# Performance work log

Measured on AMD Instinct MI355X. Metric: run time of the kernel, lower is better.

Reference implementation:

```python
import jax, jax.numpy as jnp
import numpy as np
from jax import lax

G = 64       # grid_size
K = 8        # N_knn
L = 64       # latent size
NP = 150000  # num points
NEG_SLOPE = 0.01


def lrelu(x):
    return jnp.where(x >= 0, x, NEG_SLOPE * x)


def setup_inputs() -> dict:
    key = jax.random.key(0)
    ks = jax.random.split(key, 16)
    inp = {
        "pc_KNN_pos": jax.random.normal(ks[0], (NP, K, 3), jnp.float32),
        "points": jax.random.randint(ks[1], (NP, 3), 0, G),
        # point MLP: 3 -> 64 -> 64 (LeakyReLU between)
        "W1": jax.random.normal(ks[2], (3, L), jnp.float32) * 0.3,
        "b1": jnp.zeros((L,), jnp.float32),
        "W2": jax.random.normal(ks[3], (L, L), jnp.float32) * 0.1,
        "b2": jnp.zeros((L,), jnp.float32),
        # knn aggregator: Conv1d(K,K,1) -> LeakyReLU -> Conv1d(K,1,1)
        "Wk1": jax.random.normal(ks[4], (K, K), jnp.float32) * 0.3,
        "bk1": jnp.zeros((K,), jnp.float32),
        "Wk2": jax.random.normal(ks[5], (1, K), jnp.float32) * 0.3,
        "bk2": jnp.zeros((1,), jnp.float32),
        "Cw1": jax.random.normal(ks[6], (L, L, 3, 3, 3), jnp.float32) * 0.02,
        "Cb1": jnp.zeros((L,), jnp.float32),
        "Cw2": jax.random.normal(ks[7], (L, L, 3, 3, 3), jnp.float32) * 0.02,
        "Cb2": jnp.zeros((L,), jnp.float32),
    }
    return inp


def reference(pc_KNN_pos, points, W1, b1, W2, b2, Wk1, bk1, Wk2, bk2, Cw1, Cb1, Cw2, Cb2):
    # point MLP over last dim: (Np, K, 3) -> (Np, K, L)
    h = lrelu(pc_KNN_pos @ W1 + b1)
    feat = h @ W2 + b2
    # knn_feat: 1x1 Conv1d over channel dim K (spatial dim = L)
    f1 = lrelu(jnp.einsum('ok,nkl->nol', Wk1, feat) + bk1[None, :, None])
    f2 = jnp.einsum('ok,nkl->nol', Wk2, f1) + bk2[None, :, None]  # (Np, 1, L)
    pfeat = f2[:, 0, :]  # (Np, L)
    # AvgPooling: scatter-average point features into G^3 grid cells
    idx = (points[:, 0] * G + points[:, 1]) * G + points[:, 2]  # (Np,)
    sums = jax.ops.segment_sum(pfeat, idx, num_segments=G * G * G)
    cnt = jax.ops.segment_sum(jnp.ones((pfeat.shape[0], 1), pfeat.dtype), idx,
                              num_segments=G * G * G)
    grid = jnp.where(cnt > 0, sums / jnp.maximum(cnt, 1.0), 0.0)
    grid = grid.reshape(G, G, G, L)
    # grid convs: (G,G,G,L) -> (1,L,G,G,G) -> convs -> (G,G,G,L)
    x = grid.transpose(3, 0, 1, 2)[None]
    dn = ('NCDHW', 'OIDHW', 'NCDHW')
    for w, b in ((Cw1, Cb1), (Cw2, Cb2)):
        x = lax.conv_general_dilated(x, w, (1, 1, 1), [(1, 1)] * 3,
                                     dimension_numbers=dn)
        x = jax.nn.relu(x + b[None, :, None, None, None])
    return x[0].transpose(1, 2, 3, 0)  # (G,G,G,L)
```

## Files before the change

### kernel.cpp

```cpp
#include <hip/hip_runtime.h>
#include <hip/hip_fp16.h>

#define G 64
#define KNN 8

typedef _Float16 f16x2 __attribute__((ext_vector_type(2)));
typedef _Float16 f16x8 __attribute__((ext_vector_type(8)));
typedef float f32x16 __attribute__((ext_vector_type(16)));

static __device__ __forceinline__ f16x2 pkrtz(float a, float b) {
    return __builtin_bit_cast(f16x2, __builtin_amdgcn_cvt_pkrtz(a, b));
}
static __device__ __forceinline__ void plswap(f16x2& a, f16x2& b) {
    int ai = __builtin_bit_cast(int, a), bi = __builtin_bit_cast(int, b);
    asm("v_permlane32_swap_b32 %0, %1" : "+v"(ai), "+v"(bi));
    a = __builtin_bit_cast(f16x2, ai);
    b = __builtin_bit_cast(f16x2, bi);
}

__global__ __launch_bounds__(256) void point_mlp_scatter(
    const float* __restrict__ pos, const int* __restrict__ pts,
    const float* __restrict__ W1, const float* __restrict__ b1,
    const float* __restrict__ W2, const float* __restrict__ b2,
    const float* __restrict__ Wk1, const float* __restrict__ bk1,
    const float* __restrict__ Wk2, const float* __restrict__ bk2,
    float* __restrict__ sums, float* __restrict__ cnt, int np, int nslots)
{
    __shared__ _Float16 hb[4 * 2048];

    const int tid = threadIdx.x;
    const int wv = tid >> 6;
    const int l  = tid & 63;
    const int lr = l & 31;
    const int hi = l >> 5;

    int xp = hi, yp = 2 + hi;
    asm("v_permlane32_swap_b32 %0, %1" : "+v"(xp), "+v"(yp));
    const int chan = lr + ((xp & 2) ? 32 : 0);
    const int rot = (__builtin_amdgcn_readfirstlane(xp) != 0);

    const float w1r0 = W1[l], w1r1 = W1[64 + l], w1r2 = W1[128 + l];
    const float b1v = b1[l];
    const float b2v0 = b2[lr], b2v1 = b2[32 + lr];

    f16x8 bfr[2][4];
    #pragma unroll
    for (int nf = 0; nf < 2; ++nf)
        #pragma unroll
        for (int ks = 0; ks < 4; ++ks) {
            f16x8 v;
            #pragma unroll
            for (int i = 0; i < 8; ++i)
                v[i] = (_Float16)W2[(ks * 16 + hi * 8 + i) * 64 + nf * 32 + lr];
            bfr[nf][ks] = v;
        }

    f16x2 wk1p[32];
    float bk1v[8];
    #pragma unroll
    for (int o = 0; o < 8; ++o) {
        #pragma unroll
        for (int j = 0; j < 4; ++j)
            wk1p[o * 4 + j] = f16x2{(_Float16)Wk1[o * 8 + 2 * j],
                                    (_Float16)Wk1[o * 8 + 2 * j + 1]};
        bk1v[o] = bk1[o];
    }
    f16x2 wk2p[4];
    #pragma unroll
    for (int j = 0; j < 4; ++j)
        wk2p[j] = f16x2{(_Float16)Wk2[2 * j], (_Float16)Wk2[2 * j + 1]};
    const float bk2v = bk2[0];

    _Float16* hw = hb + wv * 2048;
    const int r7 = lr & 7;

    const int ngrp = (np + 3) >> 2;
    for (int g = blockIdx.x * 4 + wv; g < ngrp; g += nslots) {
        const int gu = __builtin_amdgcn_readfirstlane(g);
        const int p0 = gu * 4;

        #pragma unroll
        for (int pl = 0; pl < 4; ++pl) {
            const float* pp = pos + (size_t)((p0 + pl < np) ? (p0 + pl) : (np - 1)) * 24;
            #pragma unroll
            for (int kk = 0; kk < KNN; ++kk) {
                const int row = pl * 8 + kk;
                float x0 = pp[kk * 3 + 0], x1 = pp[kk * 3 + 1], x2 = pp[kk * 3 + 2];
                float h = fmaf(x2, w1r2, fmaf(x1, w1r1, fmaf(x0, w1r0, b1v)));
                h = fmaxf(h, 0.01f * h);
                hw[row * 64 + (l ^ ((row & 7) << 3))] = (_Float16)h;
            }
        }

        f16x8 a[4];
        #pragma unroll
        for (int ks = 0; ks < 4; ++ks)
            a[ks] = *(const f16x8*)&hw[lr * 64 + (((ks * 2 + hi) ^ r7) << 3)];

        f32x16 acc0, acc1;
        #pragma unroll
        for (int q = 0; q < 16; ++q) { acc0[q] = 0.f; acc1[q] = 0.f; }
        #pragma unroll
        for (int ks = 0; ks < 4; ++ks) {
            acc0 = __builtin_amdgcn_mfma_f32_32x32x16_f16(a[ks], bfr[0][ks], acc0, 0, 0, 0);
            acc1 = __builtin_amdgcn_mfma_f32_32x32x16_f16(a[ks], bfr[1][ks], acc1, 0, 0, 0);
        }
        #pragma unroll
        for (int q = 0; q < 16; ++q) { acc0[q] += b2v0; acc1[q] += b2v1; }

        float pfv[4];
        #pragma unroll
        for (int pl = 0; pl < 4; ++pl) {
            f16x2 x1 = pkrtz(acc0[pl * 4 + 0], acc0[pl * 4 + 1]);
            f16x2 x2 = pkrtz(acc0[pl * 4 + 2], acc0[pl * 4 + 3]);
            f16x2 y1 = pkrtz(acc1[pl * 4 + 0], acc1[pl * 4 + 1]);
            f16x2 y2 = pkrtz(acc1[pl * 4 + 2], acc1[pl * 4 + 3]);
            plswap(x1, y1);
            plswap(x2, y2);
            f16x2 k01 = rot ? y1 : x1;
            f16x2 k23 = rot ? y2 : x2;
            f16x2 k45 = rot ? x1 : y1;
            f16x2 k67 = rot ? x2 : y2;
            float f1[8];
            #pragma unroll
            for (int o = 0; o < 8; ++o) {
                float f = bk1v[o];
                f = __builtin_amdgcn_fdot2(k01, wk1p[o * 4 + 0], f, false);
                f = __builtin_amdgcn_fdot2(k23, wk1p[o * 4 + 1], f, false);
                f = __builtin_amdgcn_fdot2(k45, wk1p[o * 4 + 2], f, false);
                f = __builtin_amdgcn_fdot2(k67, wk1p[o * 4 + 3], f, false);
                f1[o] = fmaxf(f, 0.01f * f);
            }
            float pf = bk2v;
            #pragma unroll
            for (int j = 0; j < 4; ++j)
                pf = __builtin_amdgcn_fdot2(pkrtz(f1[2 * j], f1[2 * j + 1]), wk2p[j], pf, false);
            pfv[pl] = pf;
        }

        const int* pq = pts + (size_t)p0 * 3;
        #pragma unroll
        for (int pl = 0; pl < 4; ++pl) {
            if (p0 + pl < np) {
                int cell = (pq[pl * 3 + 0] * G + pq[pl * 3 + 1]) * G + pq[pl * 3 + 2];
                atomicAdd(&sums[(size_t)cell * 64 + chan], pfv[pl]);
                if (l == 0) atomicAdd(&cnt[cell], 1.0f);
            }
        }
    }
}

__global__ __launch_bounds__(256) void transform_w_fp16(
    const float* __restrict__ w, _Float16* __restrict__ wT)
{
    int o = blockIdx.x * 256 + threadIdx.x;
    if (o < 27 * 4 * 2 * 64 * 8) {
        int i   = o & 7;
        int l   = (o >> 3) & 63;
        int nf  = (o >> 9) & 1;
        int ks  = (o >> 10) & 3;
        int tap = o >> 12;
        int co = nf * 32 + (l & 31);
        int ci = ks * 16 + (l >> 5) * 8 + i;
        wT[o] = (_Float16)w[(co * 64 + ci) * 27 + tap];
    }
}

template<int CONV1>
__global__ __launch_bounds__(256, 2) void conv3d_mfma_s(
    const void* __restrict__ in_, const float* __restrict__ cntp,
    const _Float16* __restrict__ wT, const float* __restrict__ bias,
    void* __restrict__ out_)
{
    extern __shared__ ushort tile[];

    const int lb = blockIdx.x;
    const int bx = (lb & 7) * 128 + (lb >> 3);
    const int X0 = (bx & 7) * 8, Y0 = ((bx >> 3) & 7) * 8, Z0 = (bx >> 6) * 4;
    const int tid = threadIdx.x;

    for (int c = tid; c < 4800; c += 256) {
        int vox = c >> 3, slot = c & 7;
        int hz = vox / 100, r0 = vox - hz * 100;
        int hy = r0 / 10, hx = r0 - hy * 10;
        int gz = Z0 + hz - 1, gy = Y0 + hy - 1, gx = X0 + hx - 1;
        int dst = vox * 64 + (((slot ^ hx) & 7) << 3);
        bool ok = ((unsigned)gz < 64u) && ((unsigned)gy < 64u) && ((unsigned)gx < 64u);
        if (CONV1) {
            f16x8 v;
            #pragma unroll
            for (int i = 0; i < 8; ++i) v[i] = (_Float16)0.f;
            if (ok) {
                int cell = (gz * 64 + gy) * 64 + gx;
                float cv = cntp[cell];
                float inv = (cv > 0.f) ? 1.f / cv : 0.f;
                const float4* p = (const float4*)((const float*)in_ +
                    ((size_t)cell * 64 + slot * 8));
                float4 a = p[0], b = p[1];
                v = f16x8{(_Float16)(a.x * inv), (_Float16)(a.y * inv),
                          (_Float16)(a.z * inv), (_Float16)(a.w * inv),
                          (_Float16)(b.x * inv), (_Float16)(b.y * inv),
                          (_Float16)(b.z * inv), (_Float16)(b.w * inv)};
            }
            *(f16x8*)&tile[dst] = v;
        } else {
            uint4 v = make_uint4(0u, 0u, 0u, 0u);
            if (ok) v = *(const uint4*)((const ushort*)in_ +
                    ((size_t)((gz * 64 + gy) * 64 + gx) * 64 + slot * 8));
            *(uint4*)&tile[dst] = v;
        }
    }
    __syncthreads();

    const int lane = tid & 63;
    const int wv   = tid >> 6;
    const int lr   = lane & 31;
    const int hi   = lane >> 5;

    int base_m[2];
    #pragma unroll
    for (int mt = 0; mt < 2; ++mt)
        base_m[mt] = wv * 100 + (mt * 4 + (lr >> 3)) * 10 + (lr & 7);

    f32x16 acc[2][2];
    #pragma unroll
    for (int mt = 0; mt < 2; ++mt)
        #pragma unroll
        for (int nf = 0; nf < 2; ++nf)
            #pragma unroll
            for (int q = 0; q < 16; ++q) acc[mt][nf][q] = 0.f;

    const f16x8* wTB = (const f16x8*)wT;

    #pragma unroll
    for (int dz = 0; dz < 3; ++dz)
    #pragma unroll
    for (int dy = 0; dy < 3; ++dy)
    #pragma unroll
    for (int dx = 0; dx < 3; ++dx) {
        const int tap = (dz * 3 + dy) * 3 + dx;
        const int rowoff = dz * 100 + dy * 10 + dx;
        const int sx = ((lr & 7) + dx) & 7;
        const f16x8* wB = wTB + tap * 512 + lane;
        f16x8 B0[4], B1[4];
        #pragma unroll
        for (int ks = 0; ks < 4; ++ks) {
            B0[ks] = wB[(ks * 2 + 0) * 64];
            B1[ks] = wB[(ks * 2 + 1) * 64];
        }
        #pragma unroll
        for (int ks = 0; ks < 4; ++ks) {
            const int sb = ((2 * ks + hi) ^ sx) & 7;
            #pragma unroll
            for (int mt = 0; mt < 2; ++mt) {
                int idx = (base_m[mt] + rowoff) * 64 + (sb << 3);
                f16x8 a = *(const f16x8*)&tile[idx];
                acc[mt][0] = __builtin_amdgcn_mfma_f32_32x32x16_f16(a, B0[ks], acc[mt][0], 0, 0, 0);
                acc[mt][1] = __builtin_amdgcn_mfma_f32_32x32x16_f16(a, B1[ks], acc[mt][1], 0, 0, 0);
            }
        }
    }

    const float bv0 = bias[lr], bv1 = bias[32 + lr];
    #pragma unroll
    for (int mt = 0; mt < 2; ++mt) {
        #pragma unroll
        for (int r = 0; r < 16; ++r) {
            int row = (r & 3) + 8 * (r >> 2) + 4 * hi;
            int vlw = mt * 32 + row;
            int gy = Y0 + (vlw >> 3), gx = X0 + (vlw & 7), gz = Z0 + wv;
            size_t off = (((size_t)(gz * 64 + gy) * 64 + gx) << 6) + lr;
            float v0 = fmaxf(acc[mt][0][r] + bv0, 0.f);
            float v1 = fmaxf(acc[mt][1][r] + bv1, 0.f);
            if (CONV1) {
                ((_Float16*)out_)[off]      = (_Float16)v0;
                ((_Float16*)out_)[off + 32] = (_Float16)v1;
            } else {
                ((float*)out_)[off]      = v0;
                ((float*)out_)[off + 32] = v1;
            }
        }
    }
}

extern "C" void kernel_launch(void* const* d_in, const int* in_sizes, int n_in,
                              void* d_out, int out_size, void* d_ws, size_t ws_size,
                              hipStream_t stream)
{
    const float* pos  = (const float*)d_in[0];
    const int*   pts  = (const int*)  d_in[1];
    const float* W1   = (const float*)d_in[2];
    const float* b1   = (const float*)d_in[3];
    const float* W2   = (const float*)d_in[4];
    const float* b2   = (const float*)d_in[5];
    const float* Wk1  = (const float*)d_in[6];
    const float* bk1  = (const float*)d_in[7];
    const float* Wk2  = (const float*)d_in[8];
    const float* bk2  = (const float*)d_in[9];
    const float* Cw1  = (const float*)d_in[10];
    const float* Cb1  = (const float*)d_in[11];
    const float* Cw2  = (const float*)d_in[12];
    const float* Cb2  = (const float*)d_in[13];

    float* out = (float*)d_out;
    char*  ws  = (char*)d_ws;
    _Float16* c1d  = (_Float16*)ws;
    float*    cntb = (float*)(ws + 33554432);
    _Float16* wT1  = (_Float16*)(ws + 34603008);
    _Float16* wT2  = (_Float16*)(ws + 34824192);

    const int np = in_sizes[0] / 24;

    (void)hipMemsetAsync(out,  0, 67108864, stream);
    (void)hipMemsetAsync(cntb, 0, 1048576, stream);

    transform_w_fp16<<<432, 256, 0, stream>>>(Cw1, wT1);
    transform_w_fp16<<<432, 256, 0, stream>>>(Cw2, wT2);

    const int nblk = 2048;
    point_mlp_scatter<<<nblk, 256, 0, stream>>>(
        pos, pts, W1, b1, W2, b2, Wk1, bk1, Wk2, bk2, out, cntb, np, nblk * 4);

    conv3d_mfma_s<1><<<1024, 256, 76800, stream>>>((const void*)out, cntb, wT1, Cb1, (void*)c1d);
    conv3d_mfma_s<0><<<1024, 256, 76800, stream>>>((const void*)c1d, nullptr, wT2, Cb2, (void*)out);
}
```

Baseline: 259.5 us.

## Double conv z-tile and stage input channels in two halves

The 3D conv block tile grows from 8x8x4 to 8x8x8 voxels, so each wave computes four M-tiles instead of two, and the grid shrinks to 512 blocks. To fit shared memory, the halo tile is loaded in two channel halves of 32, each followed by its own MFMA pass over the 27 taps, with a new rotation-based LDS swizzle. This cuts the halo overhead per output voxel (10x10x10 loaded for 512 outputs instead of 10x10x6 for 256). The cost is an extra synchronisation per block, more accumulator registers, and only 512 blocks, which may underfill the GPU's 256 CUs at 2 blocks per CU.

New measurement: 370.2 us. 1.43x slower.

```diff
diff --git a/kernel.cpp b/kernel.cpp
--- a/kernel.cpp
+++ b/kernel.cpp
@@ -167,7 +167,7 @@
 }
 
 template<int CONV1>
-__global__ __launch_bounds__(256, 2) void conv3d_mfma_s(
+__global__ __launch_bounds__(256, 2) void conv3d_mfma_h(
     const void* __restrict__ in_, const float* __restrict__ cntp,
     const _Float16* __restrict__ wT, const float* __restrict__ bias,
     void* __restrict__ out_)
@@ -175,56 +175,22 @@
     extern __shared__ ushort tile[];
 
     const int lb = blockIdx.x;
-    const int bx = (lb & 7) * 128 + (lb >> 3);
-    const int X0 = (bx & 7) * 8, Y0 = ((bx >> 3) & 7) * 8, Z0 = (bx >> 6) * 4;
+    const int bx = (lb & 7) * 64 + (lb >> 3);
+    const int X0 = (bx & 7) * 8, Y0 = ((bx >> 3) & 7) * 8, Z0 = (bx >> 6) * 8;
     const int tid = threadIdx.x;
-
-    for (int c = tid; c < 4800; c += 256) {
-        int vox = c >> 3, slot = c & 7;
-        int hz = vox / 100, r0 = vox - hz * 100;
-        int hy = r0 / 10, hx = r0 - hy * 10;
-        int gz = Z0 + hz - 1, gy = Y0 + hy - 1, gx = X0 + hx - 1;
-        int dst = vox * 64 + (((slot ^ hx) & 7) << 3);
-        bool ok = ((unsigned)gz < 64u) && ((unsigned)gy < 64u) && ((unsigned)gx < 64u);
-        if (CONV1) {
-            f16x8 v;
-            #pragma unroll
-            for (int i = 0; i < 8; ++i) v[i] = (_Float16)0.f;
-            if (ok) {
-                int cell = (gz * 64 + gy) * 64 + gx;
-                float cv = cntp[cell];
-                float inv = (cv > 0.f) ? 1.f / cv : 0.f;
-                const float4* p = (const float4*)((const float*)in_ +
-                    ((size_t)cell * 64 + slot * 8));
-                float4 a = p[0], b = p[1];
-                v = f16x8{(_Float16)(a.x * inv), (_Float16)(a.y * inv),
-                          (_Float16)(a.z * inv), (_Float16)(a.w * inv),
-                          (_Float16)(b.x * inv), (_Float16)(b.y * inv),
-                          (_Float16)(b.z * inv), (_Float16)(b.w * inv)};
-            }
-            *(f16x8*)&tile[dst] = v;
-        } else {
-            uint4 v = make_uint4(0u, 0u, 0u, 0u);
-            if (ok) v = *(const uint4*)((const ushort*)in_ +
-                    ((size_t)((gz * 64 + gy) * 64 + gx) * 64 + slot * 8));
-            *(uint4*)&tile[dst] = v;
-        }
-    }
-    __syncthreads();
-
     const int lane = tid & 63;
     const int wv   = tid >> 6;
     const int lr   = lane & 31;
     const int hi   = lane >> 5;
 
-    int base_m[2];
-    #pragma unroll
-    for (int mt = 0; mt < 2; ++mt)
-        base_m[mt] = wv * 100 + (mt * 4 + (lr >> 3)) * 10 + (lr & 7);
-
-    f32x16 acc[2][2];
-    #pragma unroll
-    for (int mt = 0; mt < 2; ++mt)
+    int base_m[4];
+    #pragma unroll
+    for (int mt = 0; mt < 4; ++mt)
+        base_m[mt] = (2 * wv + (mt >> 1)) * 100 + ((mt & 1) * 4 + (lr >> 3)) * 10 + (lr & 7);
+
+    f32x16 acc[4][2];
+    #pragma unroll
+    for (int mt = 0; mt < 4; ++mt)
         #pragma unroll
         for (int nf = 0; nf < 2; ++nf)
             #pragma unroll
@@ -232,43 +198,82 @@
 
     const f16x8* wTB = (const f16x8*)wT;
 
-    #pragma unroll
-    for (int dz = 0; dz < 3; ++dz)
-    #pragma unroll
-    for (int dy = 0; dy < 3; ++dy)
-    #pragma unroll
-    for (int dx = 0; dx < 3; ++dx) {
-        const int tap = (dz * 3 + dy) * 3 + dx;
-        const int rowoff = dz * 100 + dy * 10 + dx;
-        const int sx = ((lr & 7) + dx) & 7;
-        const f16x8* wB = wTB + tap * 512 + lane;
-        f16x8 B0[4], B1[4];
-        #pragma unroll
-        for (int ks = 0; ks < 4; ++ks) {
-            B0[ks] = wB[(ks * 2 + 0) * 64];
-            B1[ks] = wB[(ks * 2 + 1) * 64];
-        }
-        #pragma unroll
-        for (int ks = 0; ks < 4; ++ks) {
-            const int sb = ((2 * ks + hi) ^ sx) & 7;
-            #pragma unroll
-            for (int mt = 0; mt < 2; ++mt) {
-                int idx = (base_m[mt] + rowoff) * 64 + (sb << 3);
-                f16x8 a = *(const f16x8*)&tile[idx];
-                acc[mt][0] = __builtin_amdgcn_mfma_f32_32x32x16_f16(a, B0[ks], acc[mt][0], 0, 0, 0);
-                acc[mt][1] = __builtin_amdgcn_mfma_f32_32x32x16_f16(a, B1[ks], acc[mt][1], 0, 0, 0);
+    for (int half = 0; half < 2; ++half) {
+        if (half) __syncthreads();
+
+        for (int c = tid; c < 4000; c += 256) {
+            int vox = c >> 2, slot = c & 3;
+            int hz = vox / 100, r0 = vox - hz * 100;
+            int hy = r0 / 10, hx = r0 - hy * 10;
+            int gz = Z0 + hz - 1, gy = Y0 + hy - 1, gx = X0 + hx - 1;
+            int dst = vox * 32 + (((slot + vox) & 3) << 3);
+            bool ok = ((unsigned)gz < 64u) && ((unsigned)gy < 64u) && ((unsigned)gx < 64u);
+            if (CONV1) {
+                f16x8 v;
+                #pragma unroll
+                for (int i = 0; i < 8; ++i) v[i] = (_Float16)0.f;
+                if (ok) {
+                    int cell = (gz * 64 + gy) * 64 + gx;
+                    float cv = cntp[cell];
+                    float inv = (cv > 0.f) ? 1.f / cv : 0.f;
+                    const float4* p = (const float4*)((const float*)in_ +
+                        ((size_t)cell * 64 + half * 32 + slot * 8));
+                    float4 a = p[0], b = p[1];
+                    v = f16x8{(_Float16)(a.x * inv), (_Float16)(a.y * inv),
+                              (_Float16)(a.z * inv), (_Float16)(a.w * inv),
+                              (_Float16)(b.x * inv), (_Float16)(b.y * inv),
+                              (_Float16)(b.z * inv), (_Float16)(b.w * inv)};
+                }
+                *(f16x8*)&tile[dst] = v;
+            } else {
+                uint4 v = make_uint4(0u, 0u, 0u, 0u);
+                if (ok) v = *(const uint4*)((const ushort*)in_ +
+                        ((size_t)((gz * 64 + gy) * 64 + gx) * 64 + half * 32 + slot * 8));
+                *(uint4*)&tile[dst] = v;
+            }
+        }
+        __syncthreads();
+
+        #pragma unroll
+        for (int dz = 0; dz < 3; ++dz)
+        #pragma unroll
+        for (int dy = 0; dy < 3; ++dy)
+        #pragma unroll
+        for (int dx = 0; dx < 3; ++dx) {
+            const int tap = (dz * 3 + dy) * 3 + dx;
+            const int rowoff = dz * 100 + dy * 10 + dx;
+            const f16x8* wB = wTB + tap * 512 + lane;
+            f16x8 B0[2], B1[2];
+            #pragma unroll
+            for (int ksp = 0; ksp < 2; ++ksp) {
+                const int ks = half * 2 + ksp;
+                B0[ksp] = wB[(ks * 2 + 0) * 64];
+                B1[ksp] = wB[(ks * 2 + 1) * 64];
+            }
+            #pragma unroll
+            for (int ksp = 0; ksp < 2; ++ksp) {
+                const int c8 = ksp * 2 + hi;
+                #pragma unroll
+                for (int mt = 0; mt < 4; ++mt) {
+                    const int voxr = base_m[mt] + rowoff;
+                    f16x8 a = *(const f16x8*)&tile[voxr * 32 + (((c8 + voxr) & 3) << 3)];
+                    acc[mt][0] = __builtin_amdgcn_mfma_f32_32x32x16_f16(a, B0[ksp], acc[mt][0], 0, 0, 0);
+                    acc[mt][1] = __builtin_amdgcn_mfma_f32_32x32x16_f16(a, B1[ksp], acc[mt][1], 0, 0, 0);
+                }
             }
         }
     }
 
     const float bv0 = bias[lr], bv1 = bias[32 + lr];
     #pragma unroll
-    for (int mt = 0; mt < 2; ++mt) {
+    for (int mt = 0; mt < 4; ++mt) {
         #pragma unroll
         for (int r = 0; r < 16; ++r) {
             int row = (r & 3) + 8 * (r >> 2) + 4 * hi;
             int vlw = mt * 32 + row;
-            int gy = Y0 + (vlw >> 3), gx = X0 + (vlw & 7), gz = Z0 + wv;
+            int vz = 2 * wv + (vlw >> 6);
+            int rem = vlw & 63;
+            int gy = Y0 + (rem >> 3), gx = X0 + (rem & 7), gz = Z0 + vz;
             size_t off = (((size_t)(gz * 64 + gy) * 64 + gx) << 6) + lr;
             float v0 = fmaxf(acc[mt][0][r] + bv0, 0.f);
             float v1 = fmaxf(acc[mt][1][r] + bv1, 0.f);
@@ -321,6 +326,6 @@
     point_mlp_scatter<<<nblk, 256, 0, stream>>>(
         pos, pts, W1, b1, W2, b2, Wk1, bk1, Wk2, bk2, out, cntb, np, nblk * 4);
 
-    conv3d_mfma_s<1><<<1024, 256, 76800, stream>>>((const void*)out, cntb, wT1, Cb1, (void*)c1d);
-    conv3d_mfma_s<0><<<1024, 256, 76800, stream>>>((const void*)c1d, nullptr, wT2, Cb2, (void*)out);
-}
+    conv3d_mfma_h<1><<<512, 256, 64000, stream>>>((const void*)out, cntb, wT1, Cb1, (void*)c1d);
+    conv3d_mfma_h<0><<<512, 256, 64000, stream>>>((const void*)c1d, nullptr, wT2, Cb2, (void*)out);
+}
```
